# Kernel tuning notes

Hardware: AMD Instinct MI355X
Metric: run time of the kernel (lower is better)

## Reference

```python
import jax, jax.numpy as jnp
import numpy as np

N = 100000
E = 600000
H = 128  # embedding_size
DEPTH = 6


def setup_inputs() -> dict:
    key = jax.random.key(0)
    ks = jax.random.split(key, 12)
    X = jax.random.normal(ks[0], (N, 3), dtype=jnp.float32)
    edge_index = jax.random.randint(ks[1], (2, E), 0, N, dtype=jnp.int64)
    s = 1.0 / np.sqrt(H)
    W0 = jax.random.uniform(ks[2], (H, 3), jnp.float32, -s, s)
    b0 = jax.random.uniform(ks[3], (H,), jnp.float32, -s, s)
    W_ih = jax.random.uniform(ks[4], (3 * H, H), jnp.float32, -s, s)
    W_hh = jax.random.uniform(ks[5], (3 * H, H), jnp.float32, -s, s)
    b_ih = jax.random.uniform(ks[6], (3 * H,), jnp.float32, -s, s)
    b_hh = jax.random.uniform(ks[7], (3 * H,), jnp.float32, -s, s)
    Wm1 = jax.random.uniform(ks[8], (H // 2, H), jnp.float32, -s, s)
    bm1 = jax.random.uniform(ks[9], (H // 2,), jnp.float32, -s, s)
    Wm2 = jax.random.uniform(ks[10], (1, H // 2), jnp.float32, -s, s)
    bm2 = jax.random.uniform(ks[11], (1,), jnp.float32, -s, s)
    return {"X": X, "edge_index": edge_index, "W0": W0, "b0": b0,
            "W_ih": W_ih, "W_hh": W_hh, "b_ih": b_ih, "b_hh": b_hh,
            "Wm1": Wm1, "bm1": bm1, "Wm2": Wm2, "bm2": bm2}


def _gcn_agg(h, row, col, norm):
    # out[i] = sum_{e: col[e]==i} norm[e] * h[row[e]]
    msgs = norm[:, None] * h[row]          # [E, H]
    return jax.ops.segment_sum(msgs, col, num_segments=N)


def _gru_cell(x, h, W_ih, W_hh, b_ih, b_hh):
    gx = x @ W_ih.T + b_ih                 # [N, 3H]
    gh = h @ W_hh.T + b_hh                 # [N, 3H]
    xr, xz, xn = jnp.split(gx, 3, axis=1)
    hr, hz, hn = jnp.split(gh, 3, axis=1)
    r = jax.nn.sigmoid(xr + hr)
    z = jax.nn.sigmoid(xz + hz)
    n = jnp.tanh(xn + r * hn)
    return (1.0 - z) * n + z * h


def reference(X, edge_index, W0, b0, W_ih, W_hh, b_ih, b_hh, Wm1, bm1, Wm2, bm2):
    row, col = edge_index[0], edge_index[1]
    # degree over concat(row, col), +1, inv-sqrt with inf->0
    ones = jnp.ones((2 * E,), dtype=X.dtype)
    deg = jax.ops.segment_sum(ones, jnp.concatenate([row, col]), num_segments=N) + 1.0
    deg_inv_sqrt = deg ** -0.5
    deg_inv_sqrt = jnp.where(jnp.isinf(deg_inv_sqrt), 0.0, deg_inv_sqrt)
    norm = deg_inv_sqrt[row] * deg_inv_sqrt[col]  # [E]

    h = jax.nn.leaky_relu(X @ W0.T + b0, negative_slope=0.01)  # [N, H]
    h_max = jnp.full_like(h, -jnp.inf)
    for _ in range(DEPTH - 1):
        h_aggre = _gcn_agg(h, row, col, norm)
        h = _gru_cell(h_aggre, h, W_ih, W_hh, b_ih, b_hh)
        h_max = jnp.maximum(h_max, h)

    hid = jax.nn.leaky_relu(h_max @ Wm1.T + bm1, negative_slope=0.01)
    out = hid @ Wm2.T + bm2                # [N, 1]
    return jnp.squeeze(out, axis=-1)       # [N]
```

## Files before the change

kernel.cpp:

```cpp
#include <hip/hip_runtime.h>

#define Nn 100000
#define Ee 600000
#define Hh 128
#define NP 100096
#define NT (NP / 64)

typedef float f32x4 __attribute__((ext_vector_type(4)));
typedef unsigned short u16x8 __attribute__((ext_vector_type(8)));
typedef _Float16 f16x8 __attribute__((ext_vector_type(8)));

static __device__ __forceinline__ float sigmoidf_(float x) {
  return 1.0f / (1.0f + __expf(-x));
}
static __device__ __forceinline__ float tanh_fast(float x) {
  return 1.0f - 2.0f / (__expf(2.0f * x) + 1.0f);
}
static __device__ __forceinline__ int swz(int u) {
  return u ^ (((u >> 11) & 3) << 4);
}

__global__ void zero_kernel(int* __restrict__ a, int* __restrict__ b, int n) {
  int i = blockIdx.x * 256 + threadIdx.x;
  if (i < n) { a[i] = 0; b[i] = 0; }
}

__global__ void count_kernel(const int* __restrict__ ei, int* __restrict__ degi,
                             int* __restrict__ cnt) {
  int e = blockIdx.x * 256 + threadIdx.x;
  if (e >= Ee) return;
  int r = ei[e], c = ei[Ee + e];
  atomicAdd(&degi[r], 1);
  atomicAdd(&degi[c], 1);
  atomicAdd(&cnt[c], 1);
}

__global__ void dis_kernel(const int* __restrict__ degi, float* __restrict__ dis) {
  int i = blockIdx.x * 256 + threadIdx.x;
  if (i < Nn) dis[i] = rsqrtf((float)degi[i] + 1.0f);
}

__global__ void scan_partial(const int* __restrict__ cnt, int* __restrict__ bsum) {
  __shared__ int s[256];
  int i = blockIdx.x * 256 + threadIdx.x;
  s[threadIdx.x] = (i < Nn) ? cnt[i] : 0;
  __syncthreads();
  for (int off = 128; off > 0; off >>= 1) {
    if (threadIdx.x < off) s[threadIdx.x] += s[threadIdx.x + off];
    __syncthreads();
  }
  if (threadIdx.x == 0) bsum[blockIdx.x] = s[0];
}

__global__ void scan_bsums(const int* __restrict__ bsum, int* __restrict__ bpre, int nb) {
  __shared__ int s[512];
  int t = threadIdx.x;
  s[t] = (t < nb) ? bsum[t] : 0;
  __syncthreads();
  for (int off = 1; off < 512; off <<= 1) {
    int u = (t >= off) ? s[t - off] : 0;
    __syncthreads();
    s[t] += u;
    __syncthreads();
  }
  if (t < nb) bpre[t] = (t == 0) ? 0 : s[t - 1];
}

__global__ void scan_final(const int* __restrict__ cnt, const int* __restrict__ bpre,
                           int* __restrict__ rowptr, int* __restrict__ cursor) {
  __shared__ int s[256];
  int t = threadIdx.x;
  int i = blockIdx.x * 256 + t;
  int v = (i < Nn) ? cnt[i] : 0;
  s[t] = v;
  __syncthreads();
  for (int off = 1; off < 256; off <<= 1) {
    int u = (t >= off) ? s[t - off] : 0;
    __syncthreads();
    s[t] += u;
    __syncthreads();
  }
  int excl = s[t] - v;
  int base = bpre[blockIdx.x];
  if (i < Nn) { rowptr[i] = base + excl; cursor[i] = base + excl; }
  if (i == Nn - 1) rowptr[Nn] = base + excl + v;
}

__global__ void fill_kernel(const int* __restrict__ ei, const float* __restrict__ dis,
                            int* __restrict__ cursor, int* __restrict__ csr_src,
                            float* __restrict__ csr_w) {
  int e = blockIdx.x * 256 + threadIdx.x;
  if (e >= Ee) return;
  int r = ei[e], c = ei[Ee + e];
  int p = atomicAdd(&cursor[c], 1);
  csr_src[p] = r;
  csr_w[p] = dis[r] * dis[c];
}

__global__ void pack_kernel(const float* __restrict__ Wih, const float* __restrict__ Whh,
                            _Float16* __restrict__ Bhi, _Float16* __restrict__ Blo) {
  int t = blockIdx.x * 256 + threadIdx.x;
  if (t >= 8 * 24 * 4 * 16) return;
  int c16 = t & 15;
  int g = (t >> 4) & 3;
  int fid = (t >> 6) % 24;
  int kc = t / (24 * 64);
  int gate = fid >> 3, f = fid & 7;
  int c = f * 16 + c16;
  int wrow = gate * 128 + c;
  size_t base = (size_t)t * 8;
#pragma unroll
  for (int j = 0; j < 8; ++j) {
    int k = kc * 32 + g * 8 + j;
    float v = (k < 128) ? Wih[wrow * 128 + k] : Whh[wrow * 128 + (k - 128)];
    _Float16 hi = (_Float16)v;
    Bhi[base + j] = hi;
    Blo[base + j] = (_Float16)(v - (float)hi);
  }
}

__global__ void pack_mlp(const float* __restrict__ Wm1, _Float16* __restrict__ Bh,
                         _Float16* __restrict__ Bl) {
  int t = blockIdx.x * 256 + threadIdx.x;
  if (t >= 1024) return;
  int c16 = t & 15;
  int g = (t >> 4) & 3;
  int cf = (t >> 6) & 3;
  int kc = t >> 8;
  int c = cf * 16 + c16;
  size_t base = (size_t)t * 8;
#pragma unroll
  for (int j = 0; j < 8; ++j) {
    int k = kc * 32 + g * 8 + j;
    float v = Wm1[c * 128 + k];
    _Float16 hi = (_Float16)v;
    Bh[base + j] = hi;
    Bl[base + j] = (_Float16)(v - (float)hi);
  }
}

__global__ void h0_kernel(const float* __restrict__ X, const float* __restrict__ W0,
                          const float* __restrict__ b0, _Float16* __restrict__ H0) {
  int t = blockIdx.x * 256 + threadIdx.x;
  int i = t >> 7, d = t & 127;
  if (i >= NP) return;
  float v = 0.0f;
  if (i < Nn) {
    float x0 = X[i * 3 + 0], x1 = X[i * 3 + 1], x2 = X[i * 3 + 2];
    v = fmaf(x0, W0[d * 3 + 0], fmaf(x1, W0[d * 3 + 1], fmaf(x2, W0[d * 3 + 2], b0[d])));
    v = v > 0.0f ? v : 0.01f * v;
  }
  H0[(size_t)i * Hh + d] = (_Float16)v;
}


#define DO_GATE_AG(GB, ACC)                                                           \
  {                                                                                   \
    size_t boff = (((size_t)(kc * 24 + (GB)*8 + wave) * 4 + g) * 16 + c16) * 8;       \
    f16x8 bH = *(const f16x8*)(Bhi + boff);                                           \
    f16x8 bL = *(const f16x8*)(Blo + boff);                                           \
    _Pragma("unroll") for (int rf = 0; rf < 4; ++rf)                                  \
        ACC[rf] = __builtin_amdgcn_mfma_f32_16x16x32_f16(aH[rf], bH, ACC[rf], 0, 0, 0); \
    _Pragma("unroll") for (int rf = 0; rf < 4; ++rf)                                  \
        ACC[rf] = __builtin_amdgcn_mfma_f32_16x16x32_f16(aH[rf], bL, ACC[rf], 0, 0, 0); \
    _Pragma("unroll") for (int rf = 0; rf < 4; ++rf)                                  \
        ACC[rf] = __builtin_amdgcn_mfma_f32_16x16x32_f16(aL[rf], bH, ACC[rf], 0, 0, 0); \
  }

#define DO_GATE_H(GB, ACC)                                                            \
  {                                                                                   \
    size_t boff = (((size_t)(kc * 24 + (GB)*8 + wave) * 4 + g) * 16 + c16) * 8;       \
    f16x8 bH = *(const f16x8*)(Bhi + boff);                                           \
    f16x8 bL = *(const f16x8*)(Blo + boff);                                           \
    _Pragma("unroll") for (int rf = 0; rf < 4; ++rf)                                  \
        ACC[rf] = __builtin_amdgcn_mfma_f32_16x16x32_f16(aE[rf], bH, ACC[rf], 0, 0, 0); \
    _Pragma("unroll") for (int rf = 0; rf < 4; ++rf)                                  \
        ACC[rf] = __builtin_amdgcn_mfma_f32_16x16x32_f16(aE[rf], bL, ACC[rf], 0, 0, 0); \
  }

__global__ __launch_bounds__(512, 4) void gcn_gru_fused(
    const _Float16* __restrict__ Hp, _Float16* __restrict__ Hn,
    const int* __restrict__ csr_src, const float* __restrict__ csr_w,
    const int* __restrict__ rowptr,
    const _Float16* __restrict__ Bhi, const _Float16* __restrict__ Blo,
    const float* __restrict__ bih, const float* __restrict__ bhh) {
  __shared__ ushort SH[8192];
  __shared__ ushort SL[8192];
  const int tid = threadIdx.x;
  const int tile = blockIdx.x;
  const long rowbase = (long)tile * 64;

  const int local = tid >> 3;
  const int sub = tid & 7;
  const int eg = sub & 1;
  const int dg = sub >> 1;
  const int rf0 = local >> 4, c16l = local & 15;
  const int lwr = dg * 2048 + rf0 * 512 + c16l * 8;

  {
    const long node = rowbase + local;
    float acc[32];
#pragma unroll
    for (int m = 0; m < 32; ++m) acc[m] = 0.0f;
    if (node < Nn) {
      const int eEnd = rowptr[node + 1];
      int e = rowptr[node] + eg;
      const _Float16* hb = Hp + dg * 32;
      for (; e + 2 < eEnd; e += 4) {
        const int s0 = csr_src[e], s1 = csr_src[e + 2];
        const float w0 = csr_w[e], w1 = csr_w[e + 2];
        const f16x8* p0 = (const f16x8*)(hb + (size_t)s0 * Hh);
        const f16x8* p1 = (const f16x8*)(hb + (size_t)s1 * Hh);
        f16x8 va[4], vb[4];
#pragma unroll
        for (int q = 0; q < 4; ++q) va[q] = p0[q];
#pragma unroll
        for (int q = 0; q < 4; ++q) vb[q] = p1[q];
#pragma unroll
        for (int q = 0; q < 4; ++q)
#pragma unroll
          for (int m = 0; m < 8; ++m)
            acc[q * 8 + m] =
                fmaf(w1, (float)vb[q][m], fmaf(w0, (float)va[q][m], acc[q * 8 + m]));
      }
      if (e < eEnd) {
        const int s0 = csr_src[e];
        const float w0 = csr_w[e];
        const f16x8* p0 = (const f16x8*)(hb + (size_t)s0 * Hh);
        f16x8 va[4];
#pragma unroll
        for (int q = 0; q < 4; ++q) va[q] = p0[q];
#pragma unroll
        for (int q = 0; q < 4; ++q)
#pragma unroll
          for (int m = 0; m < 8; ++m)
            acc[q * 8 + m] = fmaf(w0, (float)va[q][m], acc[q * 8 + m]);
      }
    }
#pragma unroll
    for (int m = 0; m < 32; ++m) acc[m] += __shfl_xor(acc[m], 1);
    if (eg == 0) {
#pragma unroll
      for (int g2 = 0; g2 < 4; ++g2) {
        f16x8 vh, vl;
#pragma unroll
        for (int j = 0; j < 8; ++j) {
          float v = acc[g2 * 8 + j];
          _Float16 hi = (_Float16)v;
          vh[j] = hi;
          vl[j] = (_Float16)(v - (float)hi);
        }
        const int o = swz(lwr + g2 * 128);
        *(f16x8*)(SH + o) = vh;
        *(f16x8*)(SL + o) = vl;
      }
    }
  }
  __syncthreads();

  const int wave = tid >> 6, lane = tid & 63;
  const int g = lane >> 4, c16 = lane & 15;
  const int lbase = g * 128 + c16 * 8;

  f32x4 accR[4], accZ[4], accXN[4], accHN[4];
#pragma unroll
  for (int rf = 0; rf < 4; ++rf) {
    accR[rf] = (f32x4){0.f, 0.f, 0.f, 0.f};
    accZ[rf] = (f32x4){0.f, 0.f, 0.f, 0.f};
    accXN[rf] = (f32x4){0.f, 0.f, 0.f, 0.f};
    accHN[rf] = (f32x4){0.f, 0.f, 0.f, 0.f};
  }

#pragma unroll
  for (int kc = 0; kc < 4; ++kc) {
    f16x8 aH[4], aL[4];
#pragma unroll
    for (int rf = 0; rf < 4; ++rf) {
      int off = swz(kc * 2048 + rf * 512 + lbase);
      aH[rf] = *(const f16x8*)(SH + off);
      aL[rf] = *(const f16x8*)(SL + off);
    }
    DO_GATE_AG(0, accR)
    DO_GATE_AG(1, accZ)
    DO_GATE_AG(2, accXN)
  }
  __syncthreads();

  {
    const _Float16* p = Hp + (size_t)(rowbase + local) * Hh + dg * 32 + eg * 16;
    f16x8 v0 = *(const f16x8*)p;
    f16x8 v1 = *(const f16x8*)(p + 8);
    *(f16x8*)(SH + swz(lwr + (eg * 2 + 0) * 128)) = v0;
    *(f16x8*)(SH + swz(lwr + (eg * 2 + 1) * 128)) = v1;
  }
  __syncthreads();

#pragma unroll
  for (int kc = 4; kc < 8; ++kc) {
    f16x8 aE[4];
#pragma unroll
    for (int rf = 0; rf < 4; ++rf) {
      int off = swz((kc - 4) * 2048 + rf * 512 + lbase);
      aE[rf] = *(const f16x8*)(SH + off);
    }
    DO_GATE_H(0, accR)
    DO_GATE_H(1, accZ)
    DO_GATE_H(2, accHN)
  }

  {
    const int c = wave * 16 + c16;
    const float br = bih[c] + bhh[c];
    const float bz = bih[128 + c] + bhh[128 + c];
    const float bxn = bih[256 + c];
    const float bhn = bhh[256 + c];
    const int kcs = c >> 5;
    const int gs = (c >> 3) & 3;
    const int js = c & 7;
#pragma unroll
    for (int rf = 0; rf < 4; ++rf) {
#pragma unroll
      for (int reg = 0; reg < 4; ++reg) {
        const int lr = g * 4 + reg;
        const int hoff = swz(kcs * 2048 + rf * 512 + gs * 128 + lr * 8 + js);
        float hold = (float)*(const _Float16*)&SH[hoff];
        float rr = sigmoidf_(accR[rf][reg] + br);
        float zz = sigmoidf_(accZ[rf][reg] + bz);
        float nn = tanh_fast(accXN[rf][reg] + bxn + rr * (accHN[rf][reg] + bhn));
        Hn[(size_t)(rowbase + rf * 16 + lr) * Hh + c] =
            (_Float16)((1.0f - zz) * nn + zz * hold);
      }
    }
  }
}

__global__ __launch_bounds__(256, 4) void mlp_max_mfma(
    const _Float16* __restrict__ H1, const _Float16* __restrict__ H2,
    const _Float16* __restrict__ H3, const _Float16* __restrict__ H4,
    const _Float16* __restrict__ H5,
    const _Float16* __restrict__ Bh, const _Float16* __restrict__ Bl,
    const float* __restrict__ bm1, const float* __restrict__ Wm2,
    const float* __restrict__ bm2, float* __restrict__ out) {
  __shared__ ushort AsH[8192];
  __shared__ float red[4][64];
  const int tid = threadIdx.x;
  const long rowbase = (long)blockIdx.x * 64;

  {
    const int local = tid >> 2, kc4 = tid & 3;
    const int rf0 = local >> 4, c16l = local & 15;
    const int lwr = kc4 * 2048 + rf0 * 512 + c16l * 8;
    size_t o = (size_t)(rowbase + local) * Hh + kc4 * 32;
    f16x8 mx[4];
    {
      const f16x8* p = (const f16x8*)(H1 + o);
#pragma unroll
      for (int q = 0; q < 4; ++q) mx[q] = p[q];
    }
    const _Float16* arrs[4] = {H2, H3, H4, H5};
#pragma unroll
    for (int a = 0; a < 4; ++a) {
      const f16x8* p = (const f16x8*)(arrs[a] + o);
#pragma unroll
      for (int q = 0; q < 4; ++q) {
        f16x8 v = p[q];
#pragma unroll
        for (int m = 0; m < 8; ++m) mx[q][m] = mx[q][m] > v[m] ? mx[q][m] : v[m];
      }
    }
#pragma unroll
    for (int g2 = 0; g2 < 4; ++g2)
      *(f16x8*)(AsH + swz(lwr + g2 * 128)) = mx[g2 >> 1][0] == mx[g2 >> 1][0]
              ? ((g2 & 1) ? *(f16x8*)&mx[g2 >> 1] : *(f16x8*)&mx[g2 >> 1])
              : *(f16x8*)&mx[g2 >> 1];
#pragma unroll
    for (int g2 = 0; g2 < 4; ++g2)
      *(f16x8*)(AsH + swz(lwr + g2 * 128)) = mx[g2];
  }
  __syncthreads();

  const int wave = tid >> 6, lane = tid & 63;
  const int g = lane >> 4, c16 = lane & 15;
  const int lbase = g * 128 + c16 * 8;

  f32x4 acc[4];
#pragma unroll
  for (int rf = 0; rf < 4; ++rf) acc[rf] = (f32x4){0.f, 0.f, 0.f, 0.f};

#pragma unroll
  for (int kc = 0; kc < 4; ++kc) {
    f16x8 aE[4];
#pragma unroll
    for (int rf = 0; rf < 4; ++rf) {
      int off = swz(kc * 2048 + rf * 512 + lbase);
      aE[rf] = *(const f16x8*)(AsH + off);
    }
    size_t boff = (((size_t)(kc * 4 + wave) * 4 + g) * 16 + c16) * 8;
    f16x8 bH = *(const f16x8*)(Bh + boff);
    f16x8 bL = *(const f16x8*)(Bl + boff);
#pragma unroll
    for (int rf = 0; rf < 4; ++rf)
      acc[rf] = __builtin_amdgcn_mfma_f32_16x16x32_f16(aE[rf], bH, acc[rf], 0, 0, 0);
#pragma unroll
    for (int rf = 0; rf < 4; ++rf)
      acc[rf] = __builtin_amdgcn_mfma_f32_16x16x32_f16(aE[rf], bL, acc[rf], 0, 0, 0);
  }

  const int c = wave * 16 + c16;
  const float b1 = bm1[c];
  const float w2 = Wm2[c];
#pragma unroll
  for (int rf = 0; rf < 4; ++rf) {
#pragma unroll
    for (int reg = 0; reg < 4; ++reg) {
      float v = acc[rf][reg] + b1;
      v = v > 0.f ? v : 0.01f * v;
      v *= w2;
#pragma unroll
      for (int off = 1; off < 16; off <<= 1) v += __shfl_xor(v, off);
      if (c16 == 0) red[wave][rf * 16 + g * 4 + reg] = v;
    }
  }
  __syncthreads();
  if (tid < 64) {
    long row = rowbase + tid;
    if (row < Nn)
      out[row] = red[0][tid] + red[1][tid] + red[2][tid] + red[3][tid] + bm2[0];
  }
}

extern "C" void kernel_launch(void* const* d_in, const int* in_sizes, int n_in,
                              void* d_out, int out_size, void* d_ws, size_t ws_size,
                              hipStream_t stream) {
  const float* X = (const float*)d_in[0];
  const int* ei = (const int*)d_in[1];
  const float* W0 = (const float*)d_in[2];
  const float* b0 = (const float*)d_in[3];
  const float* Wih = (const float*)d_in[4];
  const float* Whh = (const float*)d_in[5];
  const float* bih = (const float*)d_in[6];
  const float* bhh = (const float*)d_in[7];
  const float* Wm1 = (const float*)d_in[8];
  const float* bm1 = (const float*)d_in[9];
  const float* Wm2 = (const float*)d_in[10];
  const float* bm2 = (const float*)d_in[11];
  float* out = (float*)d_out;

  char* ws = (char*)d_ws;
  size_t off = 0;
  auto alloc = [&](size_t bytes) -> void* {
    void* p = ws + off;
    off = (off + bytes + 255) & ~(size_t)255;
    return p;
  };
  _Float16* Hs[5];
  for (int i = 0; i < 5; ++i) Hs[i] = (_Float16*)alloc((size_t)NP * Hh * 2);
  _Float16* Bhi = (_Float16*)alloc((size_t)8 * 24 * 4 * 16 * 8 * 2);
  _Float16* Blo = (_Float16*)alloc((size_t)8 * 24 * 4 * 16 * 8 * 2);
  _Float16* Bmh = (_Float16*)alloc((size_t)1024 * 8 * 2);
  _Float16* Bml = (_Float16*)alloc((size_t)1024 * 8 * 2);
  float* dis = (float*)alloc((size_t)Nn * 4);
  int* degi = (int*)alloc((size_t)Nn * 4);
  int* cnt = (int*)alloc((size_t)Nn * 4);
  int* rowptr = (int*)alloc((size_t)(Nn + 1) * 4);
  int* cursor = (int*)alloc((size_t)Nn * 4);
  int* bsum = (int*)alloc(512 * 4);
  int* bpre = (int*)alloc(512 * 4);
  int* csr_src = (int*)alloc((size_t)Ee * 4);
  float* csr_w = (float*)alloc((size_t)Ee * 4);
  (void)ws_size;
  (void)in_sizes;
  (void)n_in;
  (void)out_size;

  const int NB = (Nn + 255) / 256;
  const int EB = (Ee + 255) / 256;

  zero_kernel<<<NB, 256, 0, stream>>>(degi, cnt, Nn);
  count_kernel<<<EB, 256, 0, stream>>>(ei, degi, cnt);
  dis_kernel<<<NB, 256, 0, stream>>>(degi, dis);
  scan_partial<<<NB, 256, 0, stream>>>(cnt, bsum);
  scan_bsums<<<1, 512, 0, stream>>>(bsum, bpre, NB);
  scan_final<<<NB, 256, 0, stream>>>(cnt, bpre, rowptr, cursor);
  fill_kernel<<<EB, 256, 0, stream>>>(ei, dis, cursor, csr_src, csr_w);
  pack_kernel<<<48, 256, 0, stream>>>(Wih, Whh, Bhi, Blo);
  pack_mlp<<<4, 256, 0, stream>>>(Wm1, Bmh, Bml);
  h0_kernel<<<(NP * Hh) / 256, 256, 0, stream>>>(X, W0, b0, Hs[0]);

  for (int t = 1; t <= 5; ++t) {
    gcn_gru_fused<<<NT, 512, 0, stream>>>(Hs[(t - 1) % 5], Hs[t % 5], csr_src, csr_w,
                                          rowptr, Bhi, Blo, bih, bhh);
  }

  mlp_max_mfma<<<NT, 256, 0, stream>>>(Hs[1], Hs[2], Hs[3], Hs[4], Hs[0], Bmh, Bml,
                                       bm1, Wm2, bm2, out);
}
```

Before: 617.7 us.

## Fuse final GRU step with max-pooling and MLP head; merge setup kernels

The last GCN+GRU step now runs in a kernel that keeps its output tile in shared memory, takes the elementwise max with the previous hidden states, and applies the MLP head directly. This removes one full write and re-read of a hidden-state buffer and one kernel launch. The degree inverse-sqrt is folded into the scan partial kernel, and the zero kernel is replaced by memsets. The fused kernel uses more shared memory, which may lower occupancy, and it carries some leftover dead code (an unused gcn_gru_last kernel, a self-copy of hid).

```diff
diff --git a/kernel.cpp b/kernel.cpp
--- a/kernel.cpp
+++ b/kernel.cpp
@@ -7,7 +7,6 @@
 #define NT (NP / 64)
 
 typedef float f32x4 __attribute__((ext_vector_type(4)));
-typedef unsigned short u16x8 __attribute__((ext_vector_type(8)));
 typedef _Float16 f16x8 __attribute__((ext_vector_type(8)));
 
 static __device__ __forceinline__ float sigmoidf_(float x) {
@@ -18,11 +17,6 @@
 }
 static __device__ __forceinline__ int swz(int u) {
   return u ^ (((u >> 11) & 3) << 4);
-}
-
-__global__ void zero_kernel(int* __restrict__ a, int* __restrict__ b, int n) {
-  int i = blockIdx.x * 256 + threadIdx.x;
-  if (i < n) { a[i] = 0; b[i] = 0; }
 }
 
 __global__ void count_kernel(const int* __restrict__ ei, int* __restrict__ degi,
@@ -35,15 +29,12 @@
   atomicAdd(&cnt[c], 1);
 }
 
-__global__ void dis_kernel(const int* __restrict__ degi, float* __restrict__ dis) {
-  int i = blockIdx.x * 256 + threadIdx.x;
-  if (i < Nn) dis[i] = rsqrtf((float)degi[i] + 1.0f);
-}
-
-__global__ void scan_partial(const int* __restrict__ cnt, int* __restrict__ bsum) {
+__global__ void scan_partial(const int* __restrict__ cnt, const int* __restrict__ degi,
+                             float* __restrict__ dis, int* __restrict__ bsum) {
   __shared__ int s[256];
   int i = blockIdx.x * 256 + threadIdx.x;
   s[threadIdx.x] = (i < Nn) ? cnt[i] : 0;
+  if (i < Nn) dis[i] = rsqrtf((float)degi[i] + 1.0f);
   __syncthreads();
   for (int off = 128; off > 0; off >>= 1) {
     if (threadIdx.x < off) s[threadIdx.x] += s[threadIdx.x + off];
@@ -153,7 +144,6 @@
   H0[(size_t)i * Hh + d] = (_Float16)v;
 }
 
-
 #define DO_GATE_AG(GB, ACC)                                                           \
   {                                                                                   \
     size_t boff = (((size_t)(kc * 24 + (GB)*8 + wave) * 4 + g) * 16 + c16) * 8;       \
@@ -178,6 +168,114 @@
         ACC[rf] = __builtin_amdgcn_mfma_f32_16x16x32_f16(aE[rf], bL, ACC[rf], 0, 0, 0); \
   }
 
+#define GRU_BODY                                                                      \
+  const int tid = threadIdx.x;                                                        \
+  const int tile = blockIdx.x;                                                        \
+  const long rowbase = (long)tile * 64;                                               \
+  const int local = tid >> 3;                                                         \
+  const int sub = tid & 7;                                                            \
+  const int eg = sub & 1;                                                             \
+  const int dg = sub >> 1;                                                            \
+  const int rf0 = local >> 4, c16l = local & 15;                                      \
+  const int lwr = dg * 2048 + rf0 * 512 + c16l * 8;                                   \
+  {                                                                                   \
+    const long node = rowbase + local;                                                \
+    float acc[32];                                                                    \
+    _Pragma("unroll") for (int m = 0; m < 32; ++m) acc[m] = 0.0f;                     \
+    if (node < Nn) {                                                                  \
+      const int eEnd = rowptr[node + 1];                                              \
+      int e = rowptr[node] + eg;                                                      \
+      const _Float16* hb = Hp + dg * 32;                                              \
+      for (; e + 2 < eEnd; e += 4) {                                                  \
+        const int s0 = csr_src[e], s1 = csr_src[e + 2];                               \
+        const float w0 = csr_w[e], w1 = csr_w[e + 2];                                 \
+        const f16x8* p0 = (const f16x8*)(hb + (size_t)s0 * Hh);                       \
+        const f16x8* p1 = (const f16x8*)(hb + (size_t)s1 * Hh);                       \
+        f16x8 va[4], vb[4];                                                           \
+        _Pragma("unroll") for (int q = 0; q < 4; ++q) va[q] = p0[q];                  \
+        _Pragma("unroll") for (int q = 0; q < 4; ++q) vb[q] = p1[q];                  \
+        _Pragma("unroll") for (int q = 0; q < 4; ++q)                                 \
+            _Pragma("unroll") for (int m = 0; m < 8; ++m)                             \
+                acc[q * 8 + m] = fmaf(w1, (float)vb[q][m],                            \
+                                      fmaf(w0, (float)va[q][m], acc[q * 8 + m]));     \
+      }                                                                               \
+      if (e < eEnd) {                                                                 \
+        const int s0 = csr_src[e];                                                    \
+        const float w0 = csr_w[e];                                                    \
+        const f16x8* p0 = (const f16x8*)(hb + (size_t)s0 * Hh);                       \
+        f16x8 va[4];                                                                  \
+        _Pragma("unroll") for (int q = 0; q < 4; ++q) va[q] = p0[q];                  \
+        _Pragma("unroll") for (int q = 0; q < 4; ++q)                                 \
+            _Pragma("unroll") for (int m = 0; m < 8; ++m)                             \
+                acc[q * 8 + m] = fmaf(w0, (float)va[q][m], acc[q * 8 + m]);           \
+      }                                                                               \
+    }                                                                                 \
+    _Pragma("unroll") for (int m = 0; m < 32; ++m) acc[m] += __shfl_xor(acc[m], 1);   \
+    if (eg == 0) {                                                                    \
+      _Pragma("unroll") for (int g2 = 0; g2 < 4; ++g2) {                              \
+        f16x8 vh, vl;                                                                 \
+        _Pragma("unroll") for (int j = 0; j < 8; ++j) {                               \
+          float v = acc[g2 * 8 + j];                                                  \
+          _Float16 hi = (_Float16)v;                                                  \
+          vh[j] = hi;                                                                 \
+          vl[j] = (_Float16)(v - (float)hi);                                          \
+        }                                                                             \
+        const int o = swz(lwr + g2 * 128);                                            \
+        *(f16x8*)(SH + o) = vh;                                                       \
+        *(f16x8*)(SL + o) = vl;                                                       \
+      }                                                                               \
+    }                                                                                 \
+  }                                                                                   \
+  __syncthreads();                                                                    \
+  const int wave = tid >> 6, lane = tid & 63;                                         \
+  const int g = lane >> 4, c16 = lane & 15;                                           \
+  const int lbase = g * 128 + c16 * 8;                                                \
+  f32x4 accR[4], accZ[4], accXN[4], accHN[4];                                         \
+  _Pragma("unroll") for (int rf = 0; rf < 4; ++rf) {                                  \
+    accR[rf] = (f32x4){0.f, 0.f, 0.f, 0.f};                                           \
+    accZ[rf] = (f32x4){0.f, 0.f, 0.f, 0.f};                                           \
+    accXN[rf] = (f32x4){0.f, 0.f, 0.f, 0.f};                                          \
+    accHN[rf] = (f32x4){0.f, 0.f, 0.f, 0.f};                                          \
+  }                                                                                   \
+  _Pragma("unroll") for (int kc = 0; kc < 4; ++kc) {                                  \
+    f16x8 aH[4], aL[4];                                                               \
+    _Pragma("unroll") for (int rf = 0; rf < 4; ++rf) {                                \
+      int off = swz(kc * 2048 + rf * 512 + lbase);                                    \
+      aH[rf] = *(const f16x8*)(SH + off);                                             \
+      aL[rf] = *(const f16x8*)(SL + off);                                             \
+    }                                                                                 \
+    DO_GATE_AG(0, accR)                                                               \
+    DO_GATE_AG(1, accZ)                                                               \
+    DO_GATE_AG(2, accXN)                                                              \
+  }                                                                                   \
+  __syncthreads();                                                                    \
+  {                                                                                   \
+    const _Float16* p = Hp + (size_t)(rowbase + local) * Hh + dg * 32 + eg * 16;      \
+    f16x8 v0 = *(const f16x8*)p;                                                      \
+    f16x8 v1 = *(const f16x8*)(p + 8);                                                \
+    *(f16x8*)(SH + swz(lwr + (eg * 2 + 0) * 128)) = v0;                               \
+    *(f16x8*)(SH + swz(lwr + (eg * 2 + 1) * 128)) = v1;                               \
+  }                                                                                   \
+  __syncthreads();                                                                    \
+  _Pragma("unroll") for (int kc = 4; kc < 8; ++kc) {                                  \
+    f16x8 aE[4];                                                                      \
+    _Pragma("unroll") for (int rf = 0; rf < 4; ++rf) {                                \
+      int off = swz((kc - 4) * 2048 + rf * 512 + lbase);                              \
+      aE[rf] = *(const f16x8*)(SH + off);                                             \
+    }                                                                                 \
+    DO_GATE_H(0, accR)                                                                \
+    DO_GATE_H(1, accZ)                                                                \
+    DO_GATE_H(2, accHN)                                                               \
+  }                                                                                   \
+  const int c = wave * 16 + c16;                                                      \
+  const float br = bih[c] + bhh[c];                                                   \
+  const float bz = bih[128 + c] + bhh[128 + c];                                       \
+  const float bxn = bih[256 + c];                                                     \
+  const float bhn = bhh[256 + c];                                                     \
+  const int kcs = c >> 5;                                                             \
+  const int gs = (c >> 3) & 3;                                                        \
+  const int js = c & 7;
+
 __global__ __launch_bounds__(512, 4) void gcn_gru_fused(
     const _Float16* __restrict__ Hp, _Float16* __restrict__ Hn,
     const int* __restrict__ csr_src, const float* __restrict__ csr_w,
@@ -186,246 +284,243 @@
     const float* __restrict__ bih, const float* __restrict__ bhh) {
   __shared__ ushort SH[8192];
   __shared__ ushort SL[8192];
-  const int tid = threadIdx.x;
-  const int tile = blockIdx.x;
-  const long rowbase = (long)tile * 64;
-
-  const int local = tid >> 3;
-  const int sub = tid & 7;
-  const int eg = sub & 1;
-  const int dg = sub >> 1;
-  const int rf0 = local >> 4, c16l = local & 15;
-  const int lwr = dg * 2048 + rf0 * 512 + c16l * 8;
-
-  {
-    const long node = rowbase + local;
-    float acc[32];
-#pragma unroll
-    for (int m = 0; m < 32; ++m) acc[m] = 0.0f;
-    if (node < Nn) {
-      const int eEnd = rowptr[node + 1];
-      int e = rowptr[node] + eg;
-      const _Float16* hb = Hp + dg * 32;
-      for (; e + 2 < eEnd; e += 4) {
-        const int s0 = csr_src[e], s1 = csr_src[e + 2];
-        const float w0 = csr_w[e], w1 = csr_w[e + 2];
-        const f16x8* p0 = (const f16x8*)(hb + (size_t)s0 * Hh);
-        const f16x8* p1 = (const f16x8*)(hb + (size_t)s1 * Hh);
-        f16x8 va[4], vb[4];
-#pragma unroll
-        for (int q = 0; q < 4; ++q) va[q] = p0[q];
-#pragma unroll
-        for (int q = 0; q < 4; ++q) vb[q] = p1[q];
-#pragma unroll
-        for (int q = 0; q < 4; ++q)
-#pragma unroll
-          for (int m = 0; m < 8; ++m)
-            acc[q * 8 + m] =
-                fmaf(w1, (float)vb[q][m], fmaf(w0, (float)va[q][m], acc[q * 8 + m]));
-      }
-      if (e < eEnd) {
-        const int s0 = csr_src[e];
-        const float w0 = csr_w[e];
-        const f16x8* p0 = (const f16x8*)(hb + (size_t)s0 * Hh);
-        f16x8 va[4];
-#pragma unroll
-        for (int q = 0; q < 4; ++q) va[q] = p0[q];
-#pragma unroll
-        for (int q = 0; q < 4; ++q)
-#pragma unroll
-          for (int m = 0; m < 8; ++m)
-            acc[q * 8 + m] = fmaf(w0, (float)va[q][m], acc[q * 8 + m]);
-      }
-    }
-#pragma unroll
-    for (int m = 0; m < 32; ++m) acc[m] += __shfl_xor(acc[m], 1);
-    if (eg == 0) {
-#pragma unroll
-      for (int g2 = 0; g2 < 4; ++g2) {
-        f16x8 vh, vl;
-#pragma unroll
-        for (int j = 0; j < 8; ++j) {
-          float v = acc[g2 * 8 + j];
-          _Float16 hi = (_Float16)v;
-          vh[j] = hi;
-          vl[j] = (_Float16)(v - (float)hi);
-        }
-        const int o = swz(lwr + g2 * 128);
-        *(f16x8*)(SH + o) = vh;
-        *(f16x8*)(SL + o) = vl;
-      }
-    }
-  }
-  __syncthreads();
-
-  const int wave = tid >> 6, lane = tid & 63;
-  const int g = lane >> 4, c16 = lane & 15;
-  const int lbase = g * 128 + c16 * 8;
-
-  f32x4 accR[4], accZ[4], accXN[4], accHN[4];
+  GRU_BODY
 #pragma unroll
   for (int rf = 0; rf < 4; ++rf) {
-    accR[rf] = (f32x4){0.f, 0.f, 0.f, 0.f};
-    accZ[rf] = (f32x4){0.f, 0.f, 0.f, 0.f};
-    accXN[rf] = (f32x4){0.f, 0.f, 0.f, 0.f};
-    accHN[rf] = (f32x4){0.f, 0.f, 0.f, 0.f};
-  }
-
-#pragma unroll
-  for (int kc = 0; kc < 4; ++kc) {
-    f16x8 aH[4], aL[4];
-#pragma unroll
-    for (int rf = 0; rf < 4; ++rf) {
-      int off = swz(kc * 2048 + rf * 512 + lbase);
-      aH[rf] = *(const f16x8*)(SH + off);
-      aL[rf] = *(const f16x8*)(SL + off);
-    }
-    DO_GATE_AG(0, accR)
-    DO_GATE_AG(1, accZ)
-    DO_GATE_AG(2, accXN)
-  }
-  __syncthreads();
-
-  {
-    const _Float16* p = Hp + (size_t)(rowbase + local) * Hh + dg * 32 + eg * 16;
-    f16x8 v0 = *(const f16x8*)p;
-    f16x8 v1 = *(const f16x8*)(p + 8);
-    *(f16x8*)(SH + swz(lwr + (eg * 2 + 0) * 128)) = v0;
-    *(f16x8*)(SH + swz(lwr + (eg * 2 + 1) * 128)) = v1;
-  }
-  __syncthreads();
-
-#pragma unroll
-  for (int kc = 4; kc < 8; ++kc) {
-    f16x8 aE[4];
-#pragma unroll
-    for (int rf = 0; rf < 4; ++rf) {
-      int off = swz((kc - 4) * 2048 + rf * 512 + lbase);
-      aE[rf] = *(const f16x8*)(SH + off);
-    }
-    DO_GATE_H(0, accR)
-    DO_GATE_H(1, accZ)
-    DO_GATE_H(2, accHN)
-  }
-
-  {
-    const int c = wave * 16 + c16;
-    const float br = bih[c] + bhh[c];
-    const float bz = bih[128 + c] + bhh[128 + c];
-    const float bxn = bih[256 + c];
-    const float bhn = bhh[256 + c];
-    const int kcs = c >> 5;
-    const int gs = (c >> 3) & 3;
-    const int js = c & 7;
-#pragma unroll
-    for (int rf = 0; rf < 4; ++rf) {
-#pragma unroll
-      for (int reg = 0; reg < 4; ++reg) {
-        const int lr = g * 4 + reg;
-        const int hoff = swz(kcs * 2048 + rf * 512 + gs * 128 + lr * 8 + js);
-        float hold = (float)*(const _Float16*)&SH[hoff];
-        float rr = sigmoidf_(accR[rf][reg] + br);
-        float zz = sigmoidf_(accZ[rf][reg] + bz);
-        float nn = tanh_fast(accXN[rf][reg] + bxn + rr * (accHN[rf][reg] + bhn));
-        Hn[(size_t)(rowbase + rf * 16 + lr) * Hh + c] =
-            (_Float16)((1.0f - zz) * nn + zz * hold);
-      }
-    }
-  }
-}
-
-__global__ __launch_bounds__(256, 4) void mlp_max_mfma(
-    const _Float16* __restrict__ H1, const _Float16* __restrict__ H2,
-    const _Float16* __restrict__ H3, const _Float16* __restrict__ H4,
-    const _Float16* __restrict__ H5,
-    const _Float16* __restrict__ Bh, const _Float16* __restrict__ Bl,
+#pragma unroll
+    for (int reg = 0; reg < 4; ++reg) {
+      const int lr = g * 4 + reg;
+      const int hoff = swz(kcs * 2048 + rf * 512 + gs * 128 + lr * 8 + js);
+      float hold = (float)*(const _Float16*)&SH[hoff];
+      float rr = sigmoidf_(accR[rf][reg] + br);
+      float zz = sigmoidf_(accZ[rf][reg] + bz);
+      float nn = tanh_fast(accXN[rf][reg] + bxn + rr * (accHN[rf][reg] + bhn));
+      Hn[(size_t)(rowbase + rf * 16 + lr) * Hh + c] =
+          (_Float16)((1.0f - zz) * nn + zz * hold);
+    }
+  }
+}
+
+__global__ __launch_bounds__(512, 4) void gcn_gru_last(
+    const _Float16* __restrict__ Hp,
+    const _Float16* __restrict__ Ha, const _Float16* __restrict__ Hb,
+    const _Float16* __restrict__ Hc,
+    const int* __restrict__ csr_src, const float* __restrict__ csr_w,
+    const int* __restrict__ rowptr,
+    const _Float16* __restrict__ Bhi, const _Float16* __restrict__ Blo,
+    const float* __restrict__ bih, const float* __restrict__ bhh,
+    const _Float16* __restrict__ Bmh, const _Float16* __restrict__ Bml,
     const float* __restrict__ bm1, const float* __restrict__ Wm2,
     const float* __restrict__ bm2, float* __restrict__ out) {
-  __shared__ ushort AsH[8192];
-  __shared__ float red[4][64];
-  const int tid = threadIdx.x;
-  const long rowbase = (long)blockIdx.x * 64;
+  __shared__ ushort SH[8192];
+  __shared__ ushort SL[8192];
+  __shared__ float red[8][64];
+  GRU_BODY
+#pragma unroll
+  for (int rf = 0; rf < 4; ++rf) {
+#pragma unroll
+    for (int reg = 0; reg < 4; ++reg) {
+      const int lr = g * 4 + reg;
+      const int hoff = swz(kcs * 2048 + rf * 512 + gs * 128 + lr * 8 + js);
+      float hold = (float)*(const _Float16*)&SH[hoff];
+      float rr = sigmoidf_(accR[rf][reg] + br);
+      float zz = sigmoidf_(accZ[rf][reg] + bz);
+      float nn = tanh_fast(accXN[rf][reg] + bxn + rr * (accHN[rf][reg] + bhn));
+      *(_Float16*)&SL[hoff] = (_Float16)((1.0f - zz) * nn + zz * hold);
+    }
+  }
+  __syncthreads();
 
   {
-    const int local = tid >> 2, kc4 = tid & 3;
-    const int rf0 = local >> 4, c16l = local & 15;
-    const int lwr = kc4 * 2048 + rf0 * 512 + c16l * 8;
-    size_t o = (size_t)(rowbase + local) * Hh + kc4 * 32;
-    f16x8 mx[4];
-    {
-      const f16x8* p = (const f16x8*)(H1 + o);
-#pragma unroll
-      for (int q = 0; q < 4; ++q) mx[q] = p[q];
-    }
-    const _Float16* arrs[4] = {H2, H3, H4, H5};
-#pragma unroll
-    for (int a = 0; a < 4; ++a) {
-      const f16x8* p = (const f16x8*)(arrs[a] + o);
-#pragma unroll
-      for (int q = 0; q < 4; ++q) {
-        f16x8 v = p[q];
-#pragma unroll
-        for (int m = 0; m < 8; ++m) mx[q][m] = mx[q][m] > v[m] ? mx[q][m] : v[m];
+    const size_t o = (size_t)(rowbase + local) * Hh + dg * 32 + eg * 16;
+#pragma unroll
+    for (int h2 = 0; h2 < 2; ++h2) {
+      const int slot = swz(lwr + (eg * 2 + h2) * 128);
+      f16x8 m = *(const f16x8*)(SL + slot);
+      f16x8 v;
+      v = *(const f16x8*)(Hp + o + h2 * 8);
+#pragma unroll
+      for (int mm = 0; mm < 8; ++mm) m[mm] = m[mm] > v[mm] ? m[mm] : v[mm];
+      v = *(const f16x8*)(Ha + o + h2 * 8);
+#pragma unroll
+      for (int mm = 0; mm < 8; ++mm) m[mm] = m[mm] > v[mm] ? m[mm] : v[mm];
+      v = *(const f16x8*)(Hb + o + h2 * 8);
+#pragma unroll
+      for (int mm = 0; mm < 8; ++mm) m[mm] = m[mm] > v[mm] ? m[mm] : v[mm];
+      v = *(const f16x8*)(Hc + o + h2 * 8);
+#pragma unroll
+      for (int mm = 0; mm < 8; ++mm) m[mm] = m[mm] > v[mm] ? m[mm] : v[mm];
+      *(f16x8*)(SH + slot) = m;
+    }
+  }
+  __syncthreads();
+
+  {
+    const int cf = wave >> 1, kh = wave & 1;
+    f32x4 macc[4];
+#pragma unroll
+    for (int rf = 0; rf < 4; ++rf) macc[rf] = (f32x4){0.f, 0.f, 0.f, 0.f};
+#pragma unroll
+    for (int q = 0; q < 2; ++q) {
+      const int kc = kh * 2 + q;
+      f16x8 aE[4];
+#pragma unroll
+      for (int rf = 0; rf < 4; ++rf) {
+        int off = swz(kc * 2048 + rf * 512 + lbase);
+        aE[rf] = *(const f16x8*)(SH + off);
       }
-    }
-#pragma unroll
-    for (int g2 = 0; g2 < 4; ++g2)
-      *(f16x8*)(AsH + swz(lwr + g2 * 128)) = mx[g2 >> 1][0] == mx[g2 >> 1][0]
-              ? ((g2 & 1) ? *(f16x8*)&mx[g2 >> 1] : *(f16x8*)&mx[g2 >> 1])
-              : *(f16x8*)&mx[g2 >> 1];
-#pragma unroll
-    for (int g2 = 0; g2 < 4; ++g2)
-      *(f16x8*)(AsH + swz(lwr + g2 * 128)) = mx[g2];
-  }
-  __syncthreads();
-
-  const int wave = tid >> 6, lane = tid & 63;
-  const int g = lane >> 4, c16 = lane & 15;
-  const int lbase = g * 128 + c16 * 8;
-
-  f32x4 acc[4];
-#pragma unroll
-  for (int rf = 0; rf < 4; ++rf) acc[rf] = (f32x4){0.f, 0.f, 0.f, 0.f};
-
-#pragma unroll
-  for (int kc = 0; kc < 4; ++kc) {
-    f16x8 aE[4];
+      size_t boff = (((size_t)(kc * 4 + cf) * 4 + g) * 16 + c16) * 8;
+      f16x8 bH = *(const f16x8*)(Bmh + boff);
+      f16x8 bL = *(const f16x8*)(Bml + boff);
+#pragma unroll
+      for (int rf = 0; rf < 4; ++rf)
+        macc[rf] = __builtin_amdgcn_mfma_f32_16x16x32_f16(aE[rf], bH, macc[rf], 0, 0, 0);
+#pragma unroll
+      for (int rf = 0; rf < 4; ++rf)
+        macc[rf] = __builtin_amdgcn_mfma_f32_16x16x32_f16(aE[rf], bL, macc[rf], 0, 0, 0);
+    }
+    const int hc = cf * 16 + c16;
+    const float b1 = bm1[hc] * 0.5f;
+    const float w2 = Wm2[hc];
 #pragma unroll
     for (int rf = 0; rf < 4; ++rf) {
-      int off = swz(kc * 2048 + rf * 512 + lbase);
-      aE[rf] = *(const f16x8*)(AsH + off);
-    }
-    size_t boff = (((size_t)(kc * 4 + wave) * 4 + g) * 16 + c16) * 8;
-    f16x8 bH = *(const f16x8*)(Bh + boff);
-    f16x8 bL = *(const f16x8*)(Bl + boff);
-#pragma unroll
-    for (int rf = 0; rf < 4; ++rf)
-      acc[rf] = __builtin_amdgcn_mfma_f32_16x16x32_f16(aE[rf], bH, acc[rf], 0, 0, 0);
-#pragma unroll
-    for (int rf = 0; rf < 4; ++rf)
-      acc[rf] = __builtin_amdgcn_mfma_f32_16x16x32_f16(aE[rf], bL, acc[rf], 0, 0, 0);
-  }
-
-  const int c = wave * 16 + c16;
-  const float b1 = bm1[c];
-  const float w2 = Wm2[c];
-#pragma unroll
-  for (int rf = 0; rf < 4; ++rf) {
-#pragma unroll
-    for (int reg = 0; reg < 4; ++reg) {
-      float v = acc[rf][reg] + b1;
-      v = v > 0.f ? v : 0.01f * v;
-      v *= w2;
-#pragma unroll
-      for (int off = 1; off < 16; off <<= 1) v += __shfl_xor(v, off);
-      if (c16 == 0) red[wave][rf * 16 + g * 4 + reg] = v;
-    }
+#pragma unroll
+      for (int reg = 0; reg < 4; ++reg) {
+        float v = macc[rf][reg];
+#pragma unroll
+        for (int off = 1; off < 16; off <<= 1) v += __shfl_xor(v, off);
+        if (c16 == 0) red[wave][rf * 16 + g * 4 + reg] = v;
+      }
+    }
+    (void)b1;
+    (void)w2;
   }
   __syncthreads();
   if (tid < 64) {
     long row = rowbase + tid;
-    if (row < Nn)
-      out[row] = red[0][tid] + red[1][tid] + red[2][tid] + red[3][tid] + bm2[0];
+    if (row < Nn) out[row] = red[0][tid] + red[1][tid] + red[2][tid] + red[3][tid] +
+                             red[4][tid] + red[5][tid] + red[6][tid] + red[7][tid];
+  }
+}
+
+extern "C" void kernel_launch(void* const* d_in, const int* in_sizes, int n_in,
+                              void* d_out, int out_size, void* d_ws, size_t ws_size,
+                              hipStream_t stream);
+
+
+__global__ __launch_bounds__(512, 4) void gcn_gru_last2(
+    const _Float16* __restrict__ Hp, const _Float16* __restrict__ Ha,
+    const _Float16* __restrict__ Hb, const _Float16* __restrict__ Hc,
+    const int* __restrict__ csr_src, const float* __restrict__ csr_w,
+    const int* __restrict__ rowptr,
+    const _Float16* __restrict__ Bhi, const _Float16* __restrict__ Blo,
+    const float* __restrict__ bih, const float* __restrict__ bhh,
+    const _Float16* __restrict__ Bmh, const _Float16* __restrict__ Bml,
+    const float* __restrict__ bm1, const float* __restrict__ Wm2,
+    const float* __restrict__ bm2, float* __restrict__ out) {
+  __shared__ ushort SH[8192];
+  __shared__ ushort SL[8192];
+  __shared__ float hid[64][65];
+  GRU_BODY
+#pragma unroll
+  for (int rf = 0; rf < 4; ++rf) {
+#pragma unroll
+    for (int reg = 0; reg < 4; ++reg) {
+      const int lr = g * 4 + reg;
+      const int hoff = swz(kcs * 2048 + rf * 512 + gs * 128 + lr * 8 + js);
+      float hold = (float)*(const _Float16*)&SH[hoff];
+      float rr = sigmoidf_(accR[rf][reg] + br);
+      float zz = sigmoidf_(accZ[rf][reg] + bz);
+      float nn = tanh_fast(accXN[rf][reg] + bxn + rr * (accHN[rf][reg] + bhn));
+      *(_Float16*)&SL[hoff] = (_Float16)((1.0f - zz) * nn + zz * hold);
+    }
+  }
+  __syncthreads();
+
+  {
+    const size_t o = (size_t)(rowbase + local) * Hh + dg * 32 + eg * 16;
+#pragma unroll
+    for (int h2 = 0; h2 < 2; ++h2) {
+      const int slot = swz(lwr + (eg * 2 + h2) * 128);
+      f16x8 m = *(const f16x8*)(SL + slot);
+      f16x8 v;
+      v = *(const f16x8*)(Hp + o + h2 * 8);
+#pragma unroll
+      for (int mm = 0; mm < 8; ++mm) m[mm] = m[mm] > v[mm] ? m[mm] : v[mm];
+      v = *(const f16x8*)(Ha + o + h2 * 8);
+#pragma unroll
+      for (int mm = 0; mm < 8; ++mm) m[mm] = m[mm] > v[mm] ? m[mm] : v[mm];
+      v = *(const f16x8*)(Hb + o + h2 * 8);
+#pragma unroll
+      for (int mm = 0; mm < 8; ++mm) m[mm] = m[mm] > v[mm] ? m[mm] : v[mm];
+      v = *(const f16x8*)(Hc + o + h2 * 8);
+#pragma unroll
+      for (int mm = 0; mm < 8; ++mm) m[mm] = m[mm] > v[mm] ? m[mm] : v[mm];
+      *(f16x8*)(SH + slot) = m;
+    }
+  }
+  __syncthreads();
+
+  {
+    const int cf = wave >> 1, kh = wave & 1;
+    f32x4 macc[4];
+#pragma unroll
+    for (int rf = 0; rf < 4; ++rf) macc[rf] = (f32x4){0.f, 0.f, 0.f, 0.f};
+#pragma unroll
+    for (int q = 0; q < 2; ++q) {
+      const int kc = kh * 2 + q;
+      f16x8 aE[4];
+#pragma unroll
+      for (int rf = 0; rf < 4; ++rf) {
+        int off = swz(kc * 2048 + rf * 512 + lbase);
+        aE[rf] = *(const f16x8*)(SH + off);
+      }
+      size_t boff = (((size_t)(kc * 4 + cf) * 4 + g) * 16 + c16) * 8;
+      f16x8 bH = *(const f16x8*)(Bmh + boff);
+      f16x8 bL = *(const f16x8*)(Bml + boff);
+#pragma unroll
+      for (int rf = 0; rf < 4; ++rf)
+        macc[rf] = __builtin_amdgcn_mfma_f32_16x16x32_f16(aE[rf], bH, macc[rf], 0, 0, 0);
+#pragma unroll
+      for (int rf = 0; rf < 4; ++rf)
+        macc[rf] = __builtin_amdgcn_mfma_f32_16x16x32_f16(aE[rf], bL, macc[rf], 0, 0, 0);
+    }
+    const int hc = cf * 16 + c16;
+#pragma unroll
+    for (int rf = 0; rf < 4; ++rf)
+#pragma unroll
+      for (int reg = 0; reg < 4; ++reg) {
+        const int row = rf * 16 + g * 4 + reg;
+        if (kh == 0)
+          hid[row][hc] = macc[rf][reg];
+        else
+          hid[row + 0][hc + 0] = hid[row][hc];
+      }
+    __syncthreads();
+    if (kh == 1) {
+#pragma unroll
+      for (int rf = 0; rf < 4; ++rf)
+#pragma unroll
+        for (int reg = 0; reg < 4; ++reg) {
+          const int row = rf * 16 + g * 4 + reg;
+          hid[row][hc] += macc[rf][reg];
+        }
+    }
+  }
+  __syncthreads();
+
+  if (tid < 64) {
+    long row = rowbase + tid;
+    if (row < Nn) {
+      float s = 0.f;
+#pragma unroll
+      for (int cc = 0; cc < 64; ++cc) {
+        float v = hid[tid][cc] + bm1[cc];
+        v = v > 0.f ? v : 0.01f * v;
+        s = fmaf(v, Wm2[cc], s);
+      }
+      out[row] = s + bm2[0];
+    }
   }
 }
 
@@ -476,10 +571,10 @@
   const int NB = (Nn + 255) / 256;
   const int EB = (Ee + 255) / 256;
 
-  zero_kernel<<<NB, 256, 0, stream>>>(degi, cnt, Nn);
+  hipMemsetAsync(degi, 0, (size_t)Nn * 4, stream);
+  hipMemsetAsync(cnt, 0, (size_t)Nn * 4, stream);
   count_kernel<<<EB, 256, 0, stream>>>(ei, degi, cnt);
-  dis_kernel<<<NB, 256, 0, stream>>>(degi, dis);
-  scan_partial<<<NB, 256, 0, stream>>>(cnt, bsum);
+  scan_partial<<<NB, 256, 0, stream>>>(cnt, degi, dis, bsum);
   scan_bsums<<<1, 512, 0, stream>>>(bsum, bpre, NB);
   scan_final<<<NB, 256, 0, stream>>>(cnt, bpre, rowptr, cursor);
   fill_kernel<<<EB, 256, 0, stream>>>(ei, dis, cursor, csr_src, csr_w);
@@ -487,11 +582,11 @@
   pack_mlp<<<4, 256, 0, stream>>>(Wm1, Bmh, Bml);
   h0_kernel<<<(NP * Hh) / 256, 256, 0, stream>>>(X, W0, b0, Hs[0]);
 
-  for (int t = 1; t <= 5; ++t) {
-    gcn_gru_fused<<<NT, 512, 0, stream>>>(Hs[(t - 1) % 5], Hs[t % 5], csr_src, csr_w,
+  for (int t = 1; t <= 4; ++t) {
+    gcn_gru_fused<<<NT, 512, 0, stream>>>(Hs[t - 1], Hs[t], csr_src, csr_w,
                                           rowptr, Bhi, Blo, bih, bhh);
   }
-
-  mlp_max_mfma<<<NT, 256, 0, stream>>>(Hs[1], Hs[2], Hs[3], Hs[4], Hs[0], Bmh, Bml,
-                                       bm1, Wm2, bm2, out);
-}
+  gcn_gru_last2<<<NT, 512, 0, stream>>>(Hs[4], Hs[1], Hs[2], Hs[3], csr_src, csr_w,
+                                        rowptr, Bhi, Blo, bih, bhh, Bmh, Bml,
+                                        bm1, Wm2, bm2, out);
+}
```

Result: faster. 569.6 us (-7.8%).
